# Kernel tuning notes

Hardware: AMD Instinct MI355X
Metric: run time of the kernel (lower is better)

The kernel has to match this reference:

```python
import math
import jax, jax.numpy as jnp
import numpy as np

LOG_NORM = -0.5 * math.log(2.0 * math.pi)  # per-dim gaussian normalizer
HEADS = 4
EM_ITERS = 5


def _mab(x, wq, bq, wk, bk, wv, bv, wo, bo):
    # Set-Transformer SAB(x) = MAB(x, x), ln=False
    B, S, D = x.shape
    dh = D // HEADS
    q = (x @ wq + bq).reshape(B, S, HEADS, dh)
    k = (x @ wk + bk).reshape(B, S, HEADS, dh)
    v = (x @ wv + bv).reshape(B, S, HEADS, dh)
    att = jax.nn.softmax(jnp.einsum('bqhd,bkhd->bhqk', q, k) / math.sqrt(D), axis=-1)
    o = q + jnp.einsum('bhqk,bkhd->bqhd', att, v)
    o = o.reshape(B, S, D)
    return o + jax.nn.relu(o @ wo + bo)


def setup_inputs() -> dict:
    key = jax.random.key(0)
    ks = jax.random.split(key, 16)
    B, S, D, L, K, MC = 16, 256, 512, 64, 20, 10
    s512 = 1.0 / math.sqrt(512.0)
    inp = {
        'H': jax.random.normal(ks[0], (B, S, D), jnp.float32),
        'eps': jax.random.normal(ks[1], (B * S, MC, L), jnp.float32),
        'sab_wq': jax.random.normal(ks[2], (2, D, D), jnp.float32) * s512,
        'sab_bq': jnp.zeros((2, D), jnp.float32),
        'sab_wk': jax.random.normal(ks[3], (2, D, D), jnp.float32) * s512,
        'sab_bk': jnp.zeros((2, D), jnp.float32),
        'sab_wv': jax.random.normal(ks[4], (2, D, D), jnp.float32) * s512,
        'sab_bv': jnp.zeros((2, D), jnp.float32),
        'sab_wo': jax.random.normal(ks[5], (2, D, D), jnp.float32) * s512,
        'sab_bo': jnp.zeros((2, D), jnp.float32),
        'wz': jax.random.normal(ks[6], (D, 2 * L), jnp.float32) * 0.02,
        'bz': jnp.zeros((2 * L,), jnp.float32),
        'w1': jax.random.normal(ks[7], (L, 2 * D), jnp.float32) * (1.0 / math.sqrt(L)),
        'b1': jnp.zeros((2 * D,), jnp.float32),
        'w2': jax.random.normal(ks[8], (2 * D, 2 * D), jnp.float32) * (1.0 / math.sqrt(2 * D)),
        'b2': jnp.zeros((2 * D,), jnp.float32),
        'w3': jax.random.normal(ks[9], (2 * D, D), jnp.float32) * (1.0 / math.sqrt(2 * D)),
        'b3': jnp.zeros((D,), jnp.float32),
    }
    rng = np.random.default_rng(1)
    # component_size distinct indices into the S*MC latent samples, per batch
    inp['init_idx'] = jnp.asarray(
        np.stack([rng.permutation(S * MC)[:K] for _ in range(B)]).astype(np.int32))
    return inp


def reference(H, eps, init_idx, sab_wq, sab_bq, sab_wk, sab_bk, sab_wv, sab_bv,
              sab_wo, sab_bo, wz, bz, w1, b1, w2, b2, w3, b3):
    B, S, D = H.shape
    MC, L = eps.shape[1], eps.shape[2]
    K = init_idx.shape[1]

    # q(z|x): two SABs + linear head
    h = H
    for i in range(2):
        h = _mab(h, sab_wq[i], sab_bq[i], sab_wk[i], sab_bk[i],
                 sab_wv[i], sab_bv[i], sab_wo[i], sab_bo[i])
    stats = h @ wz + bz                                    # [B,S,2L]
    mean, logvar = stats[..., :L], stats[..., L:]
    std = jnp.exp(0.5 * logvar)
    z = mean.reshape(B * S, 1, L) + eps * std.reshape(B * S, 1, L)
    z = z.reshape(B, S, MC, L)
    all_z = z.reshape(B, S * MC, L)                        # [B,N,L]

    # unsupervised EM prior (unit-variance GMM); distances via expansion
    pi = jnp.full((B, K), 1.0 / K, dtype=H.dtype)
    mu = jnp.take_along_axis(all_z, init_idx[:, :, None], axis=1)  # [B,K,L]
    x2 = jnp.sum(all_z * all_z, axis=-1)                   # [B,N]
    for _ in range(EM_ITERS):
        m2 = jnp.sum(mu * mu, axis=-1)                     # [B,K]
        ll = (-0.5 * (x2[:, :, None] - 2.0 * jnp.einsum('bnd,bkd->bnk', all_z, mu)
                      + m2[:, None, :]) + L * LOG_NORM + jnp.log(pi)[:, None, :])
        post = jax.nn.softmax(ll, axis=-1)                 # [B,N,K]
        Nk = post.sum(axis=1)                              # [B,K]
        pi = Nk / Nk.sum(axis=-1, keepdims=True)
        mu = jnp.einsum('bnk,bnd->bkd', post, all_z) / Nk[:, :, None]
    pi = jax.lax.stop_gradient(pi)
    mu = jax.lax.stop_gradient(mu)

    # reconstruction
    zf = z.reshape(-1, L)
    hr = jax.nn.relu(zf @ w1 + b1)
    hr = jax.nn.relu(hr @ w2 + b2)
    hr = jax.nn.relu(hr @ w3 + b3)
    hr = hr.reshape(B, S, MC, D)
    rec_loss = jnp.sum((hr - H[:, :, None, :]) ** 2) / (B * S * MC)

    # KL
    log_qz = jnp.sum(-0.5 * (logvar[:, :, None, :]
                             + (z - mean[:, :, None, :]) ** 2 / jnp.exp(logvar)[:, :, None, :])
                     + LOG_NORM, axis=-1)                  # [B,S,MC]
    z2 = jnp.sum(z * z, axis=-1)                           # [B,S,MC]
    m2 = jnp.sum(mu * mu, axis=-1)                         # [B,K]
    ll = (-0.5 * (z2[..., None] - 2.0 * jnp.einsum('bsmd,bkd->bsmk', z, mu)
                  + m2[:, None, None, :]) + L * LOG_NORM + jnp.log(pi)[:, None, None, :])
    log_pz = jax.scipy.special.logsumexp(ll, axis=-1)      # [B,S,MC]
    kl_loss = jnp.mean(log_qz - log_pz)
    return rec_loss, kl_loss
```

## Files before the change

kernel.cpp:

```cpp
#include <hip/hip_runtime.h>
#include <hip/hip_bf16.h>
#include <math.h>


#define BATCH 16
#define SEQ 256
#define DIM 512
#define NH 4
#define DH 128
#define LD 64
#define KC 20
#define MC 10
#define NPTS 2560
#define BS_TOT 4096
#define NROWS 40960
#define LOG_NORM (-0.9189385332046727f)

typedef __attribute__((ext_vector_type(8))) short bf16x8;
typedef __attribute__((ext_vector_type(4))) float f32x4;
typedef __hip_bfloat16 bf;

__device__ inline float warpReduceSum(float v) {
    for (int o = 32; o > 0; o >>= 1) v += __shfl_down(v, o);
    return v;
}

__device__ inline void async_copy16(const bf* g, bf* l) {
    __builtin_amdgcn_global_load_lds(
        (const __attribute__((address_space(1))) unsigned int*)g,
        (__attribute__((address_space(3))) unsigned int*)l, 16, 0, 0);
}

__device__ inline void split_store(float x, bf* ph, bf* pl, long idx) {
    const bf h = __float2bfloat16(x);
    ph[idx] = h;
    pl[idx] = __float2bfloat16(x - __bfloat162float(h));
}

template<int MODE>
__global__ __launch_bounds__(256, 3)
void gemm3t(const bf* __restrict__ Ah, const bf* __restrict__ Al,
            const bf* __restrict__ Bh, const bf* __restrict__ Bl,
            int K, int lda, int ldb,
            const float* __restrict__ b0, const float* __restrict__ b1v,
            const float* __restrict__ b2v,
            float* __restrict__ outF,
            bf* __restrict__ P1h, bf* __restrict__ P1l,
            bf* __restrict__ P2h, bf* __restrict__ P2l,
            bf* __restrict__ P3h, bf* __restrict__ P3l,
            const bf* __restrict__ Rh, const bf* __restrict__ Rl)
{
    __shared__ __align__(16) char smem[49152];
    float* Xs = (float*)smem;

    const int t = threadIdx.x;
    const int m0 = blockIdx.y * 64, n0 = blockIdx.x * 128;
    const int w = t >> 6, lane = t & 63;
    const int wn = w * 32;
    const int fm = lane & 15, quad = lane >> 4, fk = quad * 8;
    const int srow = t >> 2, scol = (t & 3) * 8;

    f32x4 acc[4][2];
#pragma unroll
    for (int i = 0; i < 4; i++)
#pragma unroll
        for (int j = 0; j < 2; j++) acc[i][j] = (f32x4){0.f, 0.f, 0.f, 0.f};

    const int nk2 = K >> 6;
    for (int kk2 = 0; kk2 < nk2; kk2++) {
#pragma unroll
        for (int h = 0; h < 2; h++) {
            const int kk = kk2 * 2 + h;
            char* base = smem + h * 24576;
            bf* Ash = (bf*)base;
            bf* Asl = (bf*)(base + 4096);
            bf* Bsh = (bf*)(base + 8192);
            bf* Bsl = (bf*)(base + 16384);
            const long ao = (long)(m0 + srow) * lda + kk * 32 + scol;
            const long bo = (long)(n0 + srow) * ldb + kk * 32 + scol;
            async_copy16(Ah + ao, Ash + w * 512);
            async_copy16(Al + ao, Asl + w * 512);
            async_copy16(Bh + bo, Bsh + w * 512);
            async_copy16(Bh + bo + 64L * ldb, Bsh + 2048 + w * 512);
            async_copy16(Bl + bo, Bsl + w * 512);
            async_copy16(Bl + bo + 64L * ldb, Bsl + 2048 + w * 512);
        }
        __syncthreads();

#pragma unroll
        for (int h = 0; h < 2; h++) {
            char* base = smem + h * 24576;
            bf* Ash = (bf*)base;
            bf* Asl = (bf*)(base + 4096);
            bf* Bsh = (bf*)(base + 8192);
            bf* Bsl = (bf*)(base + 16384);
            bf16x8 afh[4], afl[4], bfh[2], bfl[2];
#pragma unroll
            for (int mi = 0; mi < 4; mi++) {
                afh[mi] = *(const bf16x8*)&Ash[(mi * 16 + fm) * 32 + fk];
                afl[mi] = *(const bf16x8*)&Asl[(mi * 16 + fm) * 32 + fk];
            }
#pragma unroll
            for (int ni = 0; ni < 2; ni++) {
                bfh[ni] = *(const bf16x8*)&Bsh[(wn + ni * 16 + fm) * 32 + fk];
                bfl[ni] = *(const bf16x8*)&Bsl[(wn + ni * 16 + fm) * 32 + fk];
            }
#pragma unroll
            for (int mi = 0; mi < 4; mi++)
#pragma unroll
                for (int ni = 0; ni < 2; ni++) {
                    acc[mi][ni] = __builtin_amdgcn_mfma_f32_16x16x32_bf16(
                        afh[mi], bfh[ni], acc[mi][ni], 0, 0, 0);
                    acc[mi][ni] = __builtin_amdgcn_mfma_f32_16x16x32_bf16(
                        afh[mi], bfl[ni], acc[mi][ni], 0, 0, 0);
                    acc[mi][ni] = __builtin_amdgcn_mfma_f32_16x16x32_bf16(
                        afl[mi], bfh[ni], acc[mi][ni], 0, 0, 0);
                }
        }
        __syncthreads();
    }

    const int rl = t >> 2;
    const int cc4 = (t & 3) * 16;

    for (int p = 0; p < 2; p++) {
        if ((w >> 1) == p) {
            const int cb = wn - p * 64;
#pragma unroll
            for (int mi = 0; mi < 4; mi++)
#pragma unroll
                for (int ni = 0; ni < 2; ni++) {
                    const int c = cb + ni * 16 + fm;
#pragma unroll
                    for (int r = 0; r < 4; r++)
                        Xs[(mi * 16 + quad * 4 + r) * 68 + c] = acc[mi][ni][r];
                }
        }
        __syncthreads();

        if (MODE == 0 && n0 >= 1024) {
            const int hh = (n0 >> 7) & 3;
            const int dd = p * 64 + rl;
            const int bb = m0 >> 8;
            const int sb = (m0 & 255) + cc4;
            const float bias = b2v[hh * 128 + dd];
            const long ob = (((long)(bb * NH + hh) * DH + dd) << 8) + sb;
#pragma unroll
            for (int j = 0; j < 2; j++) {
                bf16x8 vh, vl;
#pragma unroll
                for (int i = 0; i < 8; i++) {
                    const float x = Xs[(cc4 + j * 8 + i) * 68 + rl] + bias;
                    const bf h = __float2bfloat16(x);
                    vh[i] = *(const short*)&h;
                    const bf l = __float2bfloat16(x - __bfloat162float(h));
                    vl[i] = *(const short*)&l;
                }
                *(bf16x8*)&P3h[ob + j * 8] = vh;
                *(bf16x8*)&P3l[ob + j * 8] = vl;
            }
        } else {
            float xv[16];
#pragma unroll
            for (int i = 0; i < 4; i++)
                *(float4*)&xv[i * 4] = *(const float4*)&Xs[rl * 68 + cc4 + i * 4];

            if (MODE == 0) {
                const int which = n0 >> 9;
                const int colq = (n0 & 511) + p * 64 + cc4;
                const float* bias = which ? b1v : b0;
                bf* Ph = which ? P2h : P1h;
                bf* Pl = which ? P2l : P1l;
                const long ob = (long)(m0 + rl) * 512 + colq;
#pragma unroll
                for (int j = 0; j < 2; j++) {
                    bf16x8 vh, vl;
#pragma unroll
                    for (int i = 0; i < 8; i++) {
                        const float x = xv[j * 8 + i] + bias[colq + j * 8 + i];
                        const bf h = __float2bfloat16(x); vh[i] = *(const short*)&h;
                        const bf l = __float2bfloat16(x - __bfloat162float(h));
                        vl[i] = *(const short*)&l;
                    }
                    *(bf16x8*)&Ph[ob + j * 8] = vh;
                    *(bf16x8*)&Pl[ob + j * 8] = vl;
                }
            } else if (MODE == 3) {
                const int colg = n0 + p * 64 + cc4;
                const long ob = (long)(m0 + rl) * 512 + colg;
#pragma unroll
                for (int j = 0; j < 2; j++) {
                    const bf16x8 rh = *(const bf16x8*)&Rh[ob + j * 8];
                    const bf16x8 rv = *(const bf16x8*)&Rl[ob + j * 8];
                    bf16x8 vh, vl;
#pragma unroll
                    for (int i = 0; i < 8; i++) {
                        short sh = rh[i], sl = rv[i];
                        float x = fmaxf(xv[j * 8 + i] + b0[colg + j * 8 + i], 0.f)
                                + __bfloat162float(*(const bf*)&sh)
                                + __bfloat162float(*(const bf*)&sl);
                        const bf h = __float2bfloat16(x); vh[i] = *(const short*)&h;
                        const bf l = __float2bfloat16(x - __bfloat162float(h));
                        vl[i] = *(const short*)&l;
                    }
                    *(bf16x8*)&P1h[ob + j * 8] = vh;
                    *(bf16x8*)&P1l[ob + j * 8] = vl;
                }
            } else {
                const int colg = p * 64 + cc4;
                const long ob = (long)(m0 + rl) * 128 + colg;
#pragma unroll
                for (int i = 0; i < 4; i++) {
                    float4 v = *(float4*)&xv[i * 4];
                    v.x += b0[colg + i * 4 + 0];
                    v.y += b0[colg + i * 4 + 1];
                    v.z += b0[colg + i * 4 + 2];
                    v.w += b0[colg + i * 4 + 3];
                    *(float4*)&outF[ob + i * 4] = v;
                }
            }
        }
        __syncthreads();
    }
}

__global__ __launch_bounds__(256)
void attn_fused(const bf* __restrict__ qh, const bf* __restrict__ ql,
                const bf* __restrict__ kh, const bf* __restrict__ kl,
                const bf* __restrict__ vTh, const bf* __restrict__ vTl,
                bf* __restrict__ oh, bf* __restrict__ ol)
{
    __shared__ __align__(16) char smem[43008];
    bf* Qsh = (bf*)smem;            bf* Qsl = (bf*)(smem + 4096);
    bf* Ksh = (bf*)(smem + 8192);   bf* Ksl = (bf*)(smem + 24576);
    bf* Psh = (bf*)smem;            bf* Psl = (bf*)(smem + 4096);
    bf* Vsh = (bf*)(smem + 8192);   bf* Vsl = (bf*)(smem + 16384);
    float (*red)[4]  = (float(*)[4])(smem + 40960);
    float (*red2)[4] = (float(*)[4])(smem + 41984);

    const int t = threadIdx.x;
    const int z = blockIdx.y;
    const int m0 = blockIdx.x * 64;
    const int bb = z >> 2, hh = z & 3;
    const long hOff = (long)bb * 131072 + (long)hh * 128;
    const long vOff = (long)z * 32768;

    const int w = t >> 6, lane = t & 63;
    const int fm = lane & 15;
    const int quad = lane >> 4;
    const int fk = quad * 8;
    const int srow = t >> 2, scol = (t & 3) * 8;

    f32x4 acc[4][4];
#pragma unroll
    for (int i = 0; i < 4; i++)
#pragma unroll
        for (int j = 0; j < 4; j++) acc[i][j] = (f32x4){0.f, 0.f, 0.f, 0.f};

    for (int kk = 0; kk < 4; kk++) {
        const long ao = hOff + (long)(m0 + srow) * 512 + kk * 32 + scol;
        const long bo = hOff + (long)srow * 512 + kk * 32 + scol;
        async_copy16(qh + ao, Qsh + w * 512);
        async_copy16(ql + ao, Qsl + w * 512);
#pragma unroll
        for (int j = 0; j < 4; j++) {
            async_copy16(kh + bo + (long)j * 64 * 512, Ksh + w * 512 + j * 2048);
            async_copy16(kl + bo + (long)j * 64 * 512, Ksl + w * 512 + j * 2048);
        }
        __syncthreads();

        bf16x8 afh[4], afl[4];
#pragma unroll
        for (int mi = 0; mi < 4; mi++) {
            afh[mi] = *(const bf16x8*)&Qsh[(mi * 16 + fm) * 32 + fk];
            afl[mi] = *(const bf16x8*)&Qsl[(mi * 16 + fm) * 32 + fk];
        }
#pragma unroll
        for (int ni = 0; ni < 4; ni++) {
            const bf16x8 bh = *(const bf16x8*)&Ksh[(w * 64 + ni * 16 + fm) * 32 + fk];
            const bf16x8 bl = *(const bf16x8*)&Ksl[(w * 64 + ni * 16 + fm) * 32 + fk];
#pragma unroll
            for (int mi = 0; mi < 4; mi++) {
                acc[mi][ni] = __builtin_amdgcn_mfma_f32_16x16x32_bf16(
                    afh[mi], bh, acc[mi][ni], 0, 0, 0);
                acc[mi][ni] = __builtin_amdgcn_mfma_f32_16x16x32_bf16(
                    afh[mi], bl, acc[mi][ni], 0, 0, 0);
                acc[mi][ni] = __builtin_amdgcn_mfma_f32_16x16x32_bf16(
                    afl[mi], bh, acc[mi][ni], 0, 0, 0);
            }
        }
        __syncthreads();
    }

    const float alpha = 0.044194173824159216f;
#pragma unroll
    for (int mi = 0; mi < 4; mi++)
#pragma unroll
        for (int r = 0; r < 4; r++) {
            float m = -1e30f;
#pragma unroll
            for (int ni = 0; ni < 4; ni++) m = fmaxf(m, acc[mi][ni][r]);
            for (int o = 8; o > 0; o >>= 1) m = fmaxf(m, __shfl_xor(m, o));
            if (fm == 0) red[mi * 16 + quad * 4 + r][w] = m;
        }
    __syncthreads();
    float invr[4][4];
#pragma unroll
    for (int mi = 0; mi < 4; mi++)
#pragma unroll
        for (int r = 0; r < 4; r++) {
            const int rowl = mi * 16 + quad * 4 + r;
            const float mx = fmaxf(fmaxf(red[rowl][0], red[rowl][1]),
                                   fmaxf(red[rowl][2], red[rowl][3]));
            float s = 0.f;
#pragma unroll
            for (int ni = 0; ni < 4; ni++) {
                const float e = __expf((acc[mi][ni][r] - mx) * alpha);
                acc[mi][ni][r] = e;
                s += e;
            }
            for (int o = 8; o > 0; o >>= 1) s += __shfl_xor(s, o);
            if (fm == 0) red2[rowl][w] = s;
        }
    __syncthreads();
#pragma unroll
    for (int mi = 0; mi < 4; mi++)
#pragma unroll
        for (int r = 0; r < 4; r++) {
            const int rowl = mi * 16 + quad * 4 + r;
            invr[mi][r] = 1.f / (red2[rowl][0] + red2[rowl][1] + red2[rowl][2] + red2[rowl][3]);
        }

    f32x4 acc2[4][2];
#pragma unroll
    for (int i = 0; i < 4; i++)
#pragma unroll
        for (int j = 0; j < 2; j++) acc2[i][j] = (f32x4){0.f, 0.f, 0.f, 0.f};

    for (int kc = 0; kc < 8; kc++) {
        if (w == (kc >> 1)) {
            const int nib = (kc & 1) * 2;
#pragma unroll
            for (int mi = 0; mi < 4; mi++)
#pragma unroll
                for (int r = 0; r < 4; r++) {
                    const int row = mi * 16 + quad * 4 + r;
#pragma unroll
                    for (int j = 0; j < 2; j++) {
                        const float p = acc[mi][nib + j][r] * invr[mi][r];
                        const int cc = j * 16 + fm;
                        const bf h = __float2bfloat16(p);
                        Psh[row * 32 + cc] = h;
                        Psl[row * 32 + cc] = __float2bfloat16(p - __bfloat162float(h));
                    }
                }
        }
        const long vo = vOff + (long)srow * 256 + kc * 32 + scol;
        async_copy16(vTh + vo, Vsh + w * 512);
        async_copy16(vTh + vo + 64L * 256, Vsh + w * 512 + 2048);
        async_copy16(vTl + vo, Vsl + w * 512);
        async_copy16(vTl + vo + 64L * 256, Vsl + w * 512 + 2048);
        __syncthreads();

        bf16x8 pfh[4], pfl[4];
#pragma unroll
        for (int mi = 0; mi < 4; mi++) {
            pfh[mi] = *(const bf16x8*)&Psh[(mi * 16 + fm) * 32 + fk];
            pfl[mi] = *(const bf16x8*)&Psl[(mi * 16 + fm) * 32 + fk];
        }
#pragma unroll
        for (int ni = 0; ni < 2; ni++) {
            const bf16x8 vh = *(const bf16x8*)&Vsh[(w * 32 + ni * 16 + fm) * 32 + fk];
            const bf16x8 vl = *(const bf16x8*)&Vsl[(w * 32 + ni * 16 + fm) * 32 + fk];
#pragma unroll
            for (int mi = 0; mi < 4; mi++) {
                acc2[mi][ni] = __builtin_amdgcn_mfma_f32_16x16x32_bf16(
                    pfh[mi], vh, acc2[mi][ni], 0, 0, 0);
                acc2[mi][ni] = __builtin_amdgcn_mfma_f32_16x16x32_bf16(
                    pfh[mi], vl, acc2[mi][ni], 0, 0, 0);
                acc2[mi][ni] = __builtin_amdgcn_mfma_f32_16x16x32_bf16(
                    pfl[mi], vh, acc2[mi][ni], 0, 0, 0);
            }
        }
        __syncthreads();
    }

#pragma unroll
    for (int ni = 0; ni < 2; ni++) {
        const int col = hh * 128 + w * 32 + ni * 16 + fm;
#pragma unroll
        for (int mi = 0; mi < 4; mi++)
#pragma unroll
            for (int r = 0; r < 4; r++) {
                const int row = mi * 16 + quad * 4 + r;
                const long idx = (long)(bb * 256 + m0 + row) * 512 + col;
                const float x = acc2[mi][ni][r]
                    + __bfloat162float(qh[idx]) + __bfloat162float(ql[idx]);
                split_store(x, oh, ol, idx);
            }
    }
}

template<bool SQLOSS>
__global__ __launch_bounds__(256, 4)
void gemm_mfma(const bf* __restrict__ A, const bf* __restrict__ BT,
               bf* __restrict__ C,
               const float* __restrict__ bias,
               const float* __restrict__ Href,
               float* __restrict__ lossAcc,
               int K, int N)
{
    __shared__ __align__(16) char smem[32768];
    bf* Cs  = (bf*)smem;
    __shared__ float redS[4];

    const int t = threadIdx.x;
    const int flat = blockIdx.y * gridDim.x + blockIdx.x;
    const int lane8 = flat & 7;
    const int grp = flat >> 3;
    const int n_blk = grp % gridDim.x;
    const int m_blk = (grp / gridDim.x) * 8 + lane8;
    const int m0 = m_blk * 128, n0 = n_blk * 128;

    const int w = t >> 6, lane = t & 63;
    const int wm = (w >> 1) * 64, wn = (w & 1) * 64;
    const int fm = lane & 15;
    const int quad = lane >> 4;
    const int fk = quad * 8;
    const int srow = t >> 2, scol = (t & 3) * 8;

    f32x4 acc[4][4];
#pragma unroll
    for (int i = 0; i < 4; i++)
#pragma unroll
        for (int j = 0; j < 4; j++) acc[i][j] = (f32x4){0.f, 0.f, 0.f, 0.f};

    const int nk2 = K >> 6;
    for (int kt2 = 0; kt2 < nk2; kt2++) {
#pragma unroll
        for (int h = 0; h < 2; h++) {
            const int kt = kt2 * 2 + h;
            bf* Asg = (bf*)(smem + h * 16384);
            bf* Bsg = (bf*)(smem + h * 16384 + 8192);
            const bf* ga = A + (long)(m0 + srow) * K + kt * 32 + scol;
            const bf* gb = BT + (long)(n0 + srow) * K + kt * 32 + scol;
            async_copy16(ga, Asg + w * 512);
            async_copy16(ga + 64L * K, Asg + 2048 + w * 512);
            async_copy16(gb, Bsg + w * 512);
            async_copy16(gb + 64L * K, Bsg + 2048 + w * 512);
        }
        __syncthreads();

#pragma unroll
        for (int h = 0; h < 2; h++) {
            bf* Asg = (bf*)(smem + h * 16384);
            bf* Bsg = (bf*)(smem + h * 16384 + 8192);
            bf16x8 af[4], bfr[4];
#pragma unroll
            for (int mi = 0; mi < 4; mi++)
                af[mi] = *(const bf16x8*)&Asg[(wm + mi * 16 + fm) * 32 + fk];
#pragma unroll
            for (int ni = 0; ni < 4; ni++)
                bfr[ni] = *(const bf16x8*)&Bsg[(wn + ni * 16 + fm) * 32 + fk];
#pragma unroll
            for (int mi = 0; mi < 4; mi++)
#pragma unroll
                for (int ni = 0; ni < 4; ni++)
                    acc[mi][ni] = __builtin_amdgcn_mfma_f32_16x16x32_bf16(
                        af[mi], bfr[ni], acc[mi][ni], 0, 0, 0);
        }
        __syncthreads();
    }

    if (SQLOSS) {
        float lsum = 0.f;
#pragma unroll
        for (int ni = 0; ni < 4; ni++) {
            const int col = n0 + wn + ni * 16 + fm;
            const float b = bias[col];
#pragma unroll
            for (int mi = 0; mi < 4; mi++)
#pragma unroll
                for (int r = 0; r < 4; r++) {
                    const int row = m0 + wm + mi * 16 + quad * 4 + r;
                    const float x = fmaxf(acc[mi][ni][r] + b, 0.f);
                    const float d = x - Href[(long)(row / MC) * DIM + col];
                    lsum = fmaf(d, d, lsum);
                }
        }
        lsum = warpReduceSum(lsum);
        if (lane == 0) redS[w] = lsum;
        __syncthreads();
        if (t == 0) atomicAdd(lossAcc, redS[0] + redS[1] + redS[2] + redS[3]);
    } else {
        for (int hf = 0; hf < 2; hf++) {
            if ((w >> 1) == hf) {
#pragma unroll
                for (int ni = 0; ni < 4; ni++) {
                    const int c = wn + ni * 16 + fm;
                    const float bv = bias[n0 + c];
#pragma unroll
                    for (int mi = 0; mi < 4; mi++)
#pragma unroll
                        for (int r = 0; r < 4; r++) {
                            const float x = fmaxf(acc[mi][ni][r] + bv, 0.f);
                            Cs[(mi * 16 + quad * 4 + r) * 136 + c] = __float2bfloat16(x);
                        }
                }
            }
            __syncthreads();
            const int rl2 = t >> 2, cc2 = (t & 3) * 32;
            const long ob = (long)(m0 + hf * 64 + rl2) * N + n0 + cc2;
#pragma unroll
            for (int j = 0; j < 4; j++)
                *(bf16x8*)&C[ob + j * 8] = *(const bf16x8*)&Cs[rl2 * 136 + cc2 + j * 8];
            __syncthreads();
        }
    }
}

__global__ __launch_bounds__(256)
void conv_all(
    const float* __restrict__ H, bf* __restrict__ h0h, bf* __restrict__ h0l,
    const float* __restrict__ wq, const float* __restrict__ wk,
    const float* __restrict__ wv, const float* __restrict__ wo,
    bf* __restrict__ qkvTh0, bf* __restrict__ qkvTl0,
    bf* __restrict__ woTh0, bf* __restrict__ woTl0,
    bf* __restrict__ qkvTh1, bf* __restrict__ qkvTl1,
    bf* __restrict__ woTh1, bf* __restrict__ woTl1,
    const float* __restrict__ wz, bf* __restrict__ wzTh, bf* __restrict__ wzTl,
    const float* __restrict__ w1, bf* __restrict__ w1T,
    const float* __restrict__ w2, bf* __restrict__ w2T,
    const float* __restrict__ w3, bf* __restrict__ w3T,
    float* __restrict__ scal, float* __restrict__ msP, float* __restrict__ nkP)
{
    __shared__ float tS[64][65];
    const int b = blockIdx.x, t = threadIdx.x;

    if (b < 2048) {
        const long base = ((long)b << 10) + (t << 2);
        const float4 v = *(const float4*)&H[base];
        ushort4 uh, ul;
        {
            const bf h0 = __float2bfloat16(v.x);
            uh.x = *(const unsigned short*)&h0;
            const bf l0 = __float2bfloat16(v.x - __bfloat162float(h0));
            ul.x = *(const unsigned short*)&l0;
        }
        {
            const bf h0 = __float2bfloat16(v.y);
            uh.y = *(const unsigned short*)&h0;
            const bf l0 = __float2bfloat16(v.y - __bfloat162float(h0));
            ul.y = *(const unsigned short*)&l0;
        }
        {
            const bf h0 = __float2bfloat16(v.z);
            uh.z = *(const unsigned short*)&h0;
            const bf l0 = __float2bfloat16(v.z - __bfloat162float(h0));
            ul.z = *(const unsigned short*)&l0;
        }
        {
            const bf h0 = __float2bfloat16(v.w);
            uh.w = *(const unsigned short*)&h0;
            const bf l0 = __float2bfloat16(v.w - __bfloat162float(h0));
            ul.w = *(const unsigned short*)&l0;
        }
        *(ushort4*)&h0h[base] = uh;
        *(ushort4*)&h0l[base] = ul;
        return;
    }
    const int bb = b - 2048;

    if (bb >= 928) {
        if (bb < 1028) {
            const long j = ((long)(bb - 928) << 10) + (t << 2);
            *(float4*)&msP[20480 + j] = (float4){0.f, 0.f, 0.f, 0.f};
        } else {
            for (int i = t; i < 1600; i += 256) nkP[320 + i] = 0.f;
            if (t < 16) scal[t] = 0.f;
        }
        return;
    }

    const float* src; bf* dH; bf* dL = nullptr;
    int Ncols, ldT, k0, n0; long dofs = 0; bool split;

    if (bb < 512) {
        const int m = bb >> 6, tile = bb & 63;
        const int layer = m >> 2, seg = m & 3;
        k0 = (tile >> 3) * 64; n0 = (tile & 7) * 64;
        src = ((seg == 0) ? wq : (seg == 1) ? wk : (seg == 2) ? wv : wo)
              + (long)layer * 262144;
        Ncols = 512; ldT = 512; split = true;
        if (seg < 3) {
            dH = layer ? qkvTh1 : qkvTh0;
            dL = layer ? qkvTl1 : qkvTl0;
            dofs = (long)seg * 262144;
        } else {
            dH = layer ? woTh1 : woTh0;
            dL = layer ? woTl1 : woTl0;
        }
    } else if (bb < 528) {
        const int i = bb - 512;
        k0 = (i >> 1) * 64; n0 = (i & 1) * 64;
        src = wz; Ncols = 128; ldT = 512; split = true;
        dH = wzTh; dL = wzTl;
    } else if (bb < 544) {
        const int i = bb - 528;
        k0 = 0; n0 = i * 64;
        src = w1; Ncols = 1024; ldT = 64; split = false;
        dH = w1T;
    } else if (bb < 800) {
        const int i = bb - 544;
        k0 = (i >> 4) * 64; n0 = (i & 15) * 64;
        src = w2; Ncols = 1024; ldT = 1024; split = false;
        dH = w2T;
    } else {
        const int i = bb - 800;
        k0 = (i >> 3) * 64; n0 = (i & 7) * 64;
        src = w3; Ncols = 512; ldT = 1024; split = false;
        dH = w3T;
    }

    {
        const int r = t >> 2, cq = (t & 3) * 16;
#pragma unroll
        for (int i = 0; i < 4; i++) {
            const float4 v = *(const float4*)&src[(long)(k0 + r) * Ncols + n0 + cq + i * 4];
            tS[r][cq + i * 4 + 0] = v.x;
            tS[r][cq + i * 4 + 1] = v.y;
            tS[r][cq + i * 4 + 2] = v.z;
            tS[r][cq + i * 4 + 3] = v.w;
        }
    }
    __syncthreads();

    {
        const int nn = t >> 2, kq = (t & 3) * 16;
        const long ob = dofs + (long)(n0 + nn) * ldT + k0 + kq;
#pragma unroll
        for (int j2 = 0; j2 < 2; j2++) {
            bf16x8 vh, vl;
#pragma unroll
            for (int j = 0; j < 8; j++) {
                const float x = tS[kq + j2 * 8 + j][nn];
                const bf h = __float2bfloat16(x);
                vh[j] = *(const short*)&h;
                const bf l = __float2bfloat16(x - __bfloat162float(h));
                vl[j] = *(const short*)&l;
            }
            *(bf16x8*)&dH[ob + j2 * 8] = vh;
            if (split) *(bf16x8*)&dL[ob + j2 * 8] = vl;
        }
    }
}

__global__ __launch_bounds__(256)
void zgen(const float* __restrict__ stats, const float* __restrict__ eps,
          float* __restrict__ z, bf* __restrict__ z16)
{
    const int idx = blockIdx.x * 256 + threadIdx.x;
    const int bs = idx / 160;
    const int r = idx % 160;
    const int l4 = r % 16;
    const float4 e = ((const float4*)eps)[idx];
    const float4 mn = ((const float4*)stats)[bs * 32 + l4];
    const float4 lv = ((const float4*)stats)[bs * 32 + 16 + l4];
    float4 zz;
    zz.x = fmaf(e.x, expf(0.5f * lv.x), mn.x);
    zz.y = fmaf(e.y, expf(0.5f * lv.y), mn.y);
    zz.z = fmaf(e.z, expf(0.5f * lv.z), mn.z);
    zz.w = fmaf(e.w, expf(0.5f * lv.w), mn.w);
    ((float4*)z)[idx] = zz;
    bf* zp = z16 + (long)idx * 4;
    zp[0] = __float2bfloat16(zz.x);
    zp[1] = __float2bfloat16(zz.y);
    zp[2] = __float2bfloat16(zz.z);
    zp[3] = __float2bfloat16(zz.w);
}

template<bool FIRST>
__global__ __launch_bounds__(256)
void em_step(const float* __restrict__ z, const int* __restrict__ init_idx,
             const float* __restrict__ msIn, const float* __restrict__ nkIn,
             float* __restrict__ msOut, float* __restrict__ nkOut)
{
    __shared__ float muS[KC][68];
    __shared__ float m2lp[KC];
    __shared__ float NkU[KC];
    __shared__ float postS[KC][256];
    __shared__ float NkS[KC];
    __shared__ float zbS[256][64];

    const int tile = blockIdx.x, b = blockIdx.y, t = threadIdx.x;
    const int lane = t & 63, w = t >> 6;

    const float* zbg = &z[((long)b * NPTS + (long)tile * 256) * LD];

    {
        const int l = t & 63, r0 = (t >> 6) * 64;
#pragma unroll 8
        for (int i = 0; i < 64; i++)
            zbS[r0 + i][l] = zbg[(r0 + i) * 64 + l];
    }

    if (t < KC) NkU[t] = FIRST ? 1.f : nkIn[b * KC + t];
    __syncthreads();
    if (FIRST) {
        for (int i = t; i < KC * LD; i += 256) {
            const int k = i >> 6, l = i & 63;
            muS[k][l] = z[((long)b * NPTS + init_idx[b * KC + k]) * LD + l];
        }
    } else {
        for (int i = t; i < KC * LD; i += 256)
            muS[i >> 6][i & 63] = msIn[b * KC * LD + i] / NkU[i >> 6];
    }
    __syncthreads();
    if (t < KC) {
        float s = 0.f;
        for (int l = 0; l < LD; l++) { const float m = muS[t][l]; s = fmaf(m, m, s); }
        float sn = 0.f;
        for (int k = 0; k < KC; k++) sn += NkU[k];
        m2lp[t] = -0.5f * s + logf(NkU[t] / sn);
    }
    __syncthreads();

    const float* zr = &zbg[(long)t * LD];
    float acc[KC];
#pragma unroll
    for (int k = 0; k < KC; k++) acc[k] = 0.f;
#pragma unroll
    for (int l4 = 0; l4 < 16; l4++) {
        const float4 zv = ((const float4*)zr)[l4];
#pragma unroll
        for (int k = 0; k < KC; k++) {
            const float4 mv = *(const float4*)&muS[k][l4 * 4];
            acc[k] = fmaf(zv.x, mv.x, acc[k]);
            acc[k] = fmaf(zv.y, mv.y, acc[k]);
            acc[k] = fmaf(zv.z, mv.z, acc[k]);
            acc[k] = fmaf(zv.w, mv.w, acc[k]);
        }
    }
    float mx = -1e30f;
    float llv[KC];
#pragma unroll
    for (int k = 0; k < KC; k++) { llv[k] = acc[k] + m2lp[k]; mx = fmaxf(mx, llv[k]); }
    float s = 0.f;
#pragma unroll
    for (int k = 0; k < KC; k++) { llv[k] = expf(llv[k] - mx); s += llv[k]; }
    const float inv = 1.f / s;
#pragma unroll
    for (int k = 0; k < KC; k++) postS[k][t] = llv[k] * inv;
    __syncthreads();

#pragma unroll
    for (int kk = 0; kk < 5; kk++) {
        const int k = w * 5 + kk;
        float p = postS[k][lane] + postS[k][lane + 64] + postS[k][lane + 128] + postS[k][lane + 192];
        p = warpReduceSum(p);
        if (lane == 0) NkS[k] = p;
    }
    __syncthreads();

#pragma unroll
    for (int j = 0; j < 5; j++) {
        const int o = t + j * 256;
        const int k = o >> 6, l = o & 63;
        float sacc = 0.f;
        for (int n2 = 0; n2 < 256; n2++)
            sacc = fmaf(postS[k][n2], zbS[n2][l], sacc);
        atomicAdd(&msOut[b * KC * LD + o], sacc);
    }
    if (t < KC) atomicAdd(&nkOut[b * KC + t], NkS[t]);
}

__global__ __launch_bounds__(256)
void kl_kernel(const float* __restrict__ z, const float* __restrict__ stats,
               const float* __restrict__ eps,
               const float* __restrict__ msIn, const float* __restrict__ nkIn,
               float* __restrict__ scal, float* __restrict__ out)
{
    __shared__ float muS[KC][68];
    __shared__ float m2lp[KC];
    __shared__ float NkU[KC];
    __shared__ float redS[4];

    const int tile = blockIdx.x, b = blockIdx.y, t = threadIdx.x;

    if (t < KC) NkU[t] = nkIn[b * KC + t];
    __syncthreads();
    for (int i = t; i < KC * LD; i += 256)
        muS[i >> 6][i & 63] = msIn[b * KC * LD + i] / NkU[i >> 6];
    __syncthreads();
    if (t < KC) {
        float s = 0.f;
        for (int l = 0; l < LD; l++) { const float m = muS[t][l]; s = fmaf(m, m, s); }
        float sn = 0.f;
        for (int k = 0; k < KC; k++) sn += NkU[k];
        m2lp[t] = -0.5f * s + logf(NkU[t] / sn);
    }
    __syncthreads();

    const int n = tile * 256 + t;
    const int sidx = n / MC, m = n % MC;
    const long bs = (long)b * SEQ + sidx;
    const float* zr = &z[((long)b * NPTS + n) * LD];

    float acc[KC];
#pragma unroll
    for (int k = 0; k < KC; k++) acc[k] = 0.f;
    float x2 = 0.f;
#pragma unroll
    for (int l4 = 0; l4 < 16; l4++) {
        const float4 zv = ((const float4*)zr)[l4];
        x2 = fmaf(zv.x, zv.x, fmaf(zv.y, zv.y, fmaf(zv.z, zv.z, fmaf(zv.w, zv.w, x2))));
#pragma unroll
        for (int k = 0; k < KC; k++) {
            const float4 mv = *(const float4*)&muS[k][l4 * 4];
            acc[k] = fmaf(zv.x, mv.x, acc[k]);
            acc[k] = fmaf(zv.y, mv.y, acc[k]);
            acc[k] = fmaf(zv.z, mv.z, acc[k]);
            acc[k] = fmaf(zv.w, mv.w, acc[k]);
        }
    }
    float mx = -1e30f;
    float llv[KC];
#pragma unroll
    for (int k = 0; k < KC; k++) { llv[k] = acc[k] + m2lp[k]; mx = fmaxf(mx, llv[k]); }
    float s = 0.f;
#pragma unroll
    for (int k = 0; k < KC; k++) s += expf(llv[k] - mx);
    const float log_pz = -0.5f * x2 + mx + logf(s) + LD * LOG_NORM;

    const float* lvr = &stats[bs * 128 + 64];
    const float* er = &eps[(bs * MC + m) * LD];
    float slv = 0.f, se2 = 0.f;
#pragma unroll
    for (int l4 = 0; l4 < 16; l4++) {
        const float4 lv = ((const float4*)lvr)[l4];
        slv += lv.x + lv.y + lv.z + lv.w;
        const float4 e = ((const float4*)er)[l4];
        se2 = fmaf(e.x, e.x, fmaf(e.y, e.y, fmaf(e.z, e.z, fmaf(e.w, e.w, se2))));
    }
    const float log_qz = -0.5f * (slv + se2) + LD * LOG_NORM;

    float v = log_qz - log_pz;
    v = warpReduceSum(v);
    if ((t & 63) == 0) redS[t >> 6] = v;
    __syncthreads();
    if (t == 0) {
        atomicAdd(&scal[1], redS[0] + redS[1] + redS[2] + redS[3]);
        __threadfence();
        const unsigned d = atomicAdd((unsigned*)&scal[2], 1u);
        if (d == 159u) {
            __threadfence();
            const float r0 = __hip_atomic_load(&scal[0], __ATOMIC_RELAXED,
                                               __HIP_MEMORY_SCOPE_AGENT);
            const float k1 = __hip_atomic_load(&scal[1], __ATOMIC_RELAXED,
                                               __HIP_MEMORY_SCOPE_AGENT);
            out[0] = r0 * (1.f / (float)NROWS);
            out[1] = k1 * (1.f / (float)NROWS);
        }
    }
}

extern "C" void kernel_launch(void* const* d_in, const int* in_sizes, int n_in,
                              void* d_out, int out_size, void* d_ws, size_t ws_size,
                              hipStream_t stream)
{
    const float* H   = (const float*)d_in[0];
    const float* eps = (const float*)d_in[1];
    const float* wq  = (const float*)d_in[2];
    const float* bq  = (const float*)d_in[3];
    const float* wk  = (const float*)d_in[4];
    const float* bk  = (const float*)d_in[5];
    const float* wv  = (const float*)d_in[6];
    const float* bv  = (const float*)d_in[7];
    const float* wo  = (const float*)d_in[8];
    const float* bo  = (const float*)d_in[9];
    const float* wz  = (const float*)d_in[10];
    const float* bz  = (const float*)d_in[11];
    const float* w1  = (const float*)d_in[12];
    const float* b1  = (const float*)d_in[13];
    const float* w2  = (const float*)d_in[14];
    const float* b2  = (const float*)d_in[15];
    const float* w3  = (const float*)d_in[16];
    const float* b3  = (const float*)d_in[17];
    const int* init_idx = (const int*)d_in[18];
    float* out = (float*)d_out;
    float* wsf = (float*)d_ws;

    const long o_scal  = 0;
    const long o_nk    = 1024;
    const long o_ms    = 4096;
    const long o_st    = 131072;
    const long o_zb    = 655360;
    const long o_z16   = 3276800;
    const long o_q     = 4587520;
    const long o_k     = 6684672;
    const long o_vT    = 8781824;
    const long o_o     = 10878976;
    const long o_h1    = 12976128;
    const long o_qkvT0 = 15073280;
    const long o_woT0  = 15859712;
    const long o_qkvT1 = 16121856;
    const long o_woT1  = 16908288;
    const long o_wzT   = 17170432;
    const long o_w1T   = 17235968;
    const long o_w2T   = 17268736;
    const long o_w3T   = 17793024;
    const long o_d1    = 18055168;
    const long o_d2    = 39026688;

    const long PL = (long)BS_TOT * DIM;
    bf* qh  = (bf*)(wsf + o_q);   bf* ql  = qh + PL;
    bf* kh  = (bf*)(wsf + o_k);   bf* kl_ = kh + PL;
    bf* vTh = (bf*)(wsf + o_vT);  bf* vTl = vTh + PL;
    bf* oh  = (bf*)(wsf + o_o);   bf* ol  = oh + PL;
    bf* h1h = (bf*)(wsf + o_h1);  bf* h1l = h1h + PL;
    bf* h2h = qh;                 bf* h2l = ql;
    bf* qkvTh0 = (bf*)(wsf + o_qkvT0); bf* qkvTl0 = qkvTh0 + 1536L * 512;
    bf* woTh0  = (bf*)(wsf + o_woT0);  bf* woTl0  = woTh0 + 512L * 512;
    bf* qkvTh1 = (bf*)(wsf + o_qkvT1); bf* qkvTl1 = qkvTh1 + 1536L * 512;
    bf* woTh1  = (bf*)(wsf + o_woT1);  bf* woTl1  = woTh1 + 512L * 512;
    bf* wzTh = (bf*)(wsf + o_wzT);     bf* wzTl = wzTh + 128L * 512;
    bf* w1T = (bf*)(wsf + o_w1T);
    bf* w2T = (bf*)(wsf + o_w2T);
    bf* w3T = (bf*)(wsf + o_w3T);
    bf* z16 = (bf*)(wsf + o_z16);
    bf* d1  = (bf*)(wsf + o_d1);
    bf* d2  = (bf*)(wsf + o_d2);
    float* st = wsf + o_st;
    float* zb = wsf + o_zb;
    float* scal = wsf + o_scal;
    float* msP = wsf + o_ms;
    float* nkP = wsf + o_nk;

    const dim3 blk(256);

    conv_all<<<3077, blk, 0, stream>>>(
        H, h1h, h1l,
        wq, wk, wv, wo,
        qkvTh0, qkvTl0, woTh0, woTl0,
        qkvTh1, qkvTl1, woTh1, woTl1,
        wz, wzTh, wzTl, w1, w1T, w2, w2T, w3, w3T,
        scal, msP, nkP);

    for (int i = 0; i < 2; i++) {
        const long boff = (long)i * DIM;
        bf* qkh = i ? qkvTh1 : qkvTh0;  bf* qkl = i ? qkvTl1 : qkvTl0;
        bf* wh  = i ? woTh1 : woTh0;    bf* wl  = i ? woTl1 : woTl0;

        gemm3t<0><<<dim3(12, 64), blk, 0, stream>>>(
            h1h, h1l, qkh, qkl, 512, 512, 512,
            bq + boff, bk + boff, bv + boff, nullptr,
            qh, ql, kh, kl_, vTh, vTl, nullptr, nullptr);
        attn_fused<<<dim3(4, 64), blk, 0, stream>>>(qh, ql, kh, kl_, vTh, vTl, oh, ol);
        bf* houth = (i == 0) ? h1h : h2h;
        bf* houtl = (i == 0) ? h1l : h2l;
        gemm3t<3><<<dim3(4, 64), blk, 0, stream>>>(
            oh, ol, wh, wl, 512, 512, 512,
            bo + boff, nullptr, nullptr, nullptr,
            houth, houtl, nullptr, nullptr, nullptr, nullptr, oh, ol);
    }

    gemm3t<4><<<dim3(1, 64), blk, 0, stream>>>(
        h2h, h2l, wzTh, wzTl, 512, 512, 512,
        bz, nullptr, nullptr, st,
        nullptr, nullptr, nullptr, nullptr, nullptr, nullptr, nullptr, nullptr);

    zgen<<<2560, blk, 0, stream>>>(st, eps, zb, z16);

    gemm_mfma<false><<<dim3(8, 320), blk, 0, stream>>>(
        z16, w1T, d1, b1, nullptr, nullptr, 64, 1024);
    gemm_mfma<false><<<dim3(8, 320), blk, 0, stream>>>(
        d1, w2T, d2, b2, nullptr, nullptr, 1024, 1024);
    gemm_mfma<true><<<dim3(4, 320), blk, 0, stream>>>(
        d2, w3T, nullptr, b3, H, scal + 0, 1024, 512);

    em_step<true><<<dim3(10, 16), blk, 0, stream>>>(
        zb, init_idx, nullptr, nullptr,
        msP + 1L * 16 * KC * LD, nkP + 1L * 16 * KC);
    for (int it = 1; it < 5; it++) {
        em_step<false><<<dim3(10, 16), blk, 0, stream>>>(
            zb, nullptr,
            msP + (long)it * 16 * KC * LD, nkP + (long)it * 16 * KC,
            msP + (long)(it + 1) * 16 * KC * LD, nkP + (long)(it + 1) * 16 * KC);
    }
    kl_kernel<<<dim3(10, 16), blk, 0, stream>>>(
        zb, st, eps,
        msP + 5L * 16 * KC * LD, nkP + 5L * 16 * KC, scal, out);
}
```

Baseline: 618.7 us.

## Stage all attention P tiles in LDS up front and vectorize EM z loads

```diff
diff --git a/kernel.cpp b/kernel.cpp
--- a/kernel.cpp
+++ b/kernel.cpp
@@ -230,13 +230,15 @@
                 const bf* __restrict__ vTh, const bf* __restrict__ vTl,
                 bf* __restrict__ oh, bf* __restrict__ ol)
 {
-    __shared__ __align__(16) char smem[43008];
+    __shared__ __align__(16) char smem[124928];
     bf* Qsh = (bf*)smem;            bf* Qsl = (bf*)(smem + 4096);
     bf* Ksh = (bf*)(smem + 8192);   bf* Ksl = (bf*)(smem + 24576);
-    bf* Psh = (bf*)smem;            bf* Psl = (bf*)(smem + 4096);
-    bf* Vsh = (bf*)(smem + 8192);   bf* Vsl = (bf*)(smem + 16384);
     float (*red)[4]  = (float(*)[4])(smem + 40960);
     float (*red2)[4] = (float(*)[4])(smem + 41984);
+    bf* PhB = (bf*)(smem + 43008);
+    bf* PlB = (bf*)(smem + 75776);
+    bf* Vsh = (bf*)(smem + 108544);
+    bf* Vsl = (bf*)(smem + 116736);
 
     const int t = threadIdx.x;
     const int z = blockIdx.y;
@@ -331,6 +333,27 @@
             invr[mi][r] = 1.f / (red2[rowl][0] + red2[rowl][1] + red2[rowl][2] + red2[rowl][3]);
         }
 
+#pragma unroll
+    for (int half = 0; half < 2; half++) {
+        bf* Ph = PhB + (2 * w + half) * 2048;
+        bf* Pl = PlB + (2 * w + half) * 2048;
+        const int nib = half * 2;
+#pragma unroll
+        for (int mi = 0; mi < 4; mi++)
+#pragma unroll
+            for (int r = 0; r < 4; r++) {
+                const int row = mi * 16 + quad * 4 + r;
+#pragma unroll
+                for (int j = 0; j < 2; j++) {
+                    const float p = acc[mi][nib + j][r] * invr[mi][r];
+                    const int cc = j * 16 + fm;
+                    const bf h = __float2bfloat16(p);
+                    Ph[row * 32 + cc] = h;
+                    Pl[row * 32 + cc] = __float2bfloat16(p - __bfloat162float(h));
+                }
+            }
+    }
+
     f32x4 acc2[4][2];
 #pragma unroll
     for (int i = 0; i < 4; i++)
@@ -338,23 +361,6 @@
         for (int j = 0; j < 2; j++) acc2[i][j] = (f32x4){0.f, 0.f, 0.f, 0.f};
 
     for (int kc = 0; kc < 8; kc++) {
-        if (w == (kc >> 1)) {
-            const int nib = (kc & 1) * 2;
-#pragma unroll
-            for (int mi = 0; mi < 4; mi++)
-#pragma unroll
-                for (int r = 0; r < 4; r++) {
-                    const int row = mi * 16 + quad * 4 + r;
-#pragma unroll
-                    for (int j = 0; j < 2; j++) {
-                        const float p = acc[mi][nib + j][r] * invr[mi][r];
-                        const int cc = j * 16 + fm;
-                        const bf h = __float2bfloat16(p);
-                        Psh[row * 32 + cc] = h;
-                        Psl[row * 32 + cc] = __float2bfloat16(p - __bfloat162float(h));
-                    }
-                }
-        }
         const long vo = vOff + (long)srow * 256 + kc * 32 + scol;
         async_copy16(vTh + vo, Vsh + w * 512);
         async_copy16(vTh + vo + 64L * 256, Vsh + w * 512 + 2048);
@@ -362,11 +368,13 @@
         async_copy16(vTl + vo + 64L * 256, Vsl + w * 512 + 2048);
         __syncthreads();
 
+        const bf* Psh_k = PhB + kc * 2048;
+        const bf* Psl_k = PlB + kc * 2048;
         bf16x8 pfh[4], pfl[4];
 #pragma unroll
         for (int mi = 0; mi < 4; mi++) {
-            pfh[mi] = *(const bf16x8*)&Psh[(mi * 16 + fm) * 32 + fk];
-            pfl[mi] = *(const bf16x8*)&Psl[(mi * 16 + fm) * 32 + fk];
+            pfh[mi] = *(const bf16x8*)&Psh_k[(mi * 16 + fm) * 32 + fk];
+            pfl[mi] = *(const bf16x8*)&Psl_k[(mi * 16 + fm) * 32 + fk];
         }
 #pragma unroll
         for (int ni = 0; ni < 2; ni++) {
@@ -698,10 +706,13 @@
     const float* zbg = &z[((long)b * NPTS + (long)tile * 256) * LD];
 
     {
-        const int l = t & 63, r0 = (t >> 6) * 64;
-#pragma unroll 8
-        for (int i = 0; i < 64; i++)
-            zbS[r0 + i][l] = zbg[(r0 + i) * 64 + l];
+        const int c4 = (t & 15) * 4;
+        const int r0 = t >> 4;
+#pragma unroll
+        for (int p = 0; p < 16; p++) {
+            const int r = r0 + p * 16;
+            *(float4*)&zbS[r][c4] = *(const float4*)&zbg[(long)r * 64 + c4];
+        }
     }
 
     if (t < KC) NkU[t] = FIRST ? 1.f : nkIn[b * KC + t];
```

After: 633.6 us. +2.4%, slower.
